# Optimization experiments

Measured on AMD Instinct MI355X. Metric: run time of the kernel, lower is better.

The kernel has to match this reference:

```python
import jax, jax.numpy as jnp
import numpy as np

DIM = 1024
HEADS = 16
DIM_HEAD = 64
INNER = HEADS * DIM_HEAD  # 1024
MLP = 4096
EPS = 1e-5


def setup_inputs() -> dict:
    key = jax.random.key(0)
    ks = jax.random.split(key, 8)
    s = lambda fan_in: 1.0 / np.sqrt(fan_in)
    return {
        "x": jax.random.normal(ks[0], (4, 2048, DIM), dtype=jnp.float32),
        "ln1_g": jnp.ones((DIM,), jnp.float32),
        "ln1_b": jnp.zeros((DIM,), jnp.float32),
        "w_qkv": jax.random.normal(ks[1], (DIM, 3 * INNER), jnp.float32) * s(DIM),
        "w_out": jax.random.normal(ks[2], (INNER, DIM), jnp.float32) * s(INNER),
        "b_out": jnp.zeros((DIM,), jnp.float32),
        "ln2_g": jnp.ones((DIM,), jnp.float32),
        "ln2_b": jnp.zeros((DIM,), jnp.float32),
        "w1": jax.random.normal(ks[3], (DIM, MLP), jnp.float32) * s(DIM),
        "b1": jnp.zeros((MLP,), jnp.float32),
        "w2": jax.random.normal(ks[4], (MLP, DIM), jnp.float32) * s(MLP),
        "b2": jnp.zeros((DIM,), jnp.float32),
    }


def _layernorm(x, g, b):
    mu = jnp.mean(x, axis=-1, keepdims=True)
    var = jnp.mean(jnp.square(x - mu), axis=-1, keepdims=True)
    return (x - mu) * jax.lax.rsqrt(var + EPS) * g + b


def _block(x, ln1_g, ln1_b, w_qkv, w_out, b_out, ln2_g, ln2_b, w1, b1, w2, b2):
    # pre-norm attention
    h = _layernorm(x, ln1_g, ln1_b)
    qkv = h @ w_qkv  # [b, n, 3*inner]
    q, k, v = jnp.split(qkv, 3, axis=-1)
    def heads(t):  # b n (h d) -> b h n d
        b, n, _ = t.shape
        return t.reshape(b, n, HEADS, DIM_HEAD).transpose(0, 2, 1, 3)
    q, k, v = heads(q), heads(k), heads(v)
    scale = DIM_HEAD ** -0.5
    dots = jnp.einsum("bhnd,bhmd->bhnm", q, k) * scale
    attn = jax.nn.softmax(dots, axis=-1)
    out = jnp.einsum("bhnm,bhmd->bhnd", attn, v)
    b, _, n, _ = out.shape
    out = out.transpose(0, 2, 1, 3).reshape(b, n, INNER)
    x = out @ w_out + b_out + x
    # pre-norm FFN
    h = _layernorm(x, ln2_g, ln2_b)
    h = jax.nn.gelu(h @ w1 + b1, approximate=False)
    return h @ w2 + b2 + x


def reference(x, ln1_g, ln1_b, w_qkv, w_out, b_out, ln2_g, ln2_b, w1, b1, w2, b2):
    return _block(x, ln1_g, ln1_b, w_qkv, w_out, b_out, ln2_g, ln2_b, w1, b1, w2, b2)
```

## Files before the change

kernel.cpp:

```cpp
#include <hip/hip_runtime.h>
#include <hip/hip_bf16.h>
#include <math.h>


typedef __bf16 bf16;
typedef __bf16 bf16x8 __attribute__((ext_vector_type(8)));
typedef __bf16 bf16x4 __attribute__((ext_vector_type(4)));
typedef float  f32x4  __attribute__((ext_vector_type(4)));
typedef unsigned int u32;

#define MFMA_16x16x32(a, b, c) __builtin_amdgcn_mfma_f32_16x16x32_bf16((a), (b), (c), 0, 0, 0)

__device__ __forceinline__ void gl_lds16(const void* g, void* l) {
    __builtin_amdgcn_global_load_lds(
        (const __attribute__((address_space(1))) u32*)g,
        (__attribute__((address_space(3))) u32*)l, 16, 0, 0);
}

__device__ __forceinline__ float fast_gelu(float x) {
    const float u = x * (0.7978845608028654f + 0.03567740814183f * x * x);
    const float e = __builtin_amdgcn_exp2f(u * 2.8853900817779268f);
    return x * e * __builtin_amdgcn_rcpf(e + 1.0f);
}

__global__ __launch_bounds__(256) void transpose_f32_bf16(
    const float* __restrict__ in, bf16* __restrict__ out, int R, int C)
{
    __shared__ float tile[32][33];
    const int cb = blockIdx.x * 32, rb = blockIdx.y * 32;
    const int c = threadIdx.x & 31, r0 = threadIdx.x >> 5;
#pragma unroll
    for (int i = 0; i < 4; ++i) {
        int r = r0 + i * 8;
        tile[r][c] = in[(size_t)(rb + r) * C + cb + c];
    }
    __syncthreads();
#pragma unroll
    for (int i = 0; i < 4; ++i) {
        int rr = r0 + i * 8;
        out[(size_t)(cb + rr) * R + rb + c] = (bf16)tile[c][rr];
    }
}

__global__ __launch_bounds__(256) void transpose_v(
    const bf16* __restrict__ qkv, bf16* __restrict__ VT)
{
    __shared__ float tile[32][33];
    const int tokb = blockIdx.x * 32;
    const int db   = blockIdx.y * 32;
    const int bh   = blockIdx.z;
    const int b = bh >> 4, h = bh & 15;
    const int c = threadIdx.x & 31, r0 = threadIdx.x >> 5;
#pragma unroll
    for (int i = 0; i < 4; ++i) {
        int r = r0 + i * 8;
        tile[r][c] = (float)qkv[(size_t)(b * 2048 + tokb + r) * 3072 + 2048 + h * 64 + db + c];
    }
    __syncthreads();
#pragma unroll
    for (int i = 0; i < 4; ++i) {
        int rr = r0 + i * 8;
        VT[((size_t)bh * 64 + db + rr) * 2048 + tokb + c] = (bf16)tile[c][rr];
    }
}

__global__ __launch_bounds__(256) void ln_kernel(
    const float* __restrict__ x, const float* __restrict__ g,
    const float* __restrict__ b, bf16* __restrict__ out)
{
    const int lane = threadIdx.x & 63;
    const int wv   = threadIdx.x >> 6;
    const size_t token = (size_t)blockIdx.x * 4 + wv;
    const float* xr = x + token * 1024;
    float4 v[4];
    float s = 0.f, ss = 0.f;
#pragma unroll
    for (int c = 0; c < 4; ++c) {
        v[c] = *(const float4*)(xr + c * 256 + lane * 4);
        s  += v[c].x + v[c].y + v[c].z + v[c].w;
        ss += v[c].x * v[c].x + v[c].y * v[c].y + v[c].z * v[c].z + v[c].w * v[c].w;
    }
#pragma unroll
    for (int off = 32; off > 0; off >>= 1) {
        s  += __shfl_xor(s, off);
        ss += __shfl_xor(ss, off);
    }
    const float mu  = s * (1.0f / 1024.0f);
    const float var = ss * (1.0f / 1024.0f) - mu * mu;
    const float rs  = rsqrtf(var + 1e-5f);
    bf16* orow = out + token * 1024;
#pragma unroll
    for (int c = 0; c < 4; ++c) {
        float4 gg = *(const float4*)(g + c * 256 + lane * 4);
        float4 bb = *(const float4*)(b + c * 256 + lane * 4);
        bf16x4 o;
        o[0] = (bf16)((v[c].x - mu) * rs * gg.x + bb.x);
        o[1] = (bf16)((v[c].y - mu) * rs * gg.y + bb.y);
        o[2] = (bf16)((v[c].z - mu) * rs * gg.z + bb.z);
        o[3] = (bf16)((v[c].w - mu) * rs * gg.w + bb.w);
        *(bf16x4*)(orow + c * 256 + lane * 4) = o;
    }
}

template <int EPI>
__global__ __launch_bounds__(256, 4) void gemm_bt(
    const bf16* __restrict__ A, const bf16* __restrict__ Bt,
    const float* __restrict__ bias, const float* __restrict__ resid,
    void* __restrict__ outp, int M, int N, int K)
{
    __shared__ __align__(16) bf16 sA[128 * 64];
    __shared__ __align__(16) bf16 sB[128 * 64];

    const int tid  = threadIdx.x;
    const int lane = tid & 63;
    const int wv   = tid >> 6;
    const int quad = lane >> 4;
    const int l16  = lane & 15;

    const int id  = blockIdx.x;
    const int xcd = id & 7, j = id >> 3;
    const int M0 = (xcd * 8 + (j & 7)) * 128;
    const int N0 = (j >> 3) * 128;

    const int wm = (wv >> 1) * 64;
    const int wn = (wv & 1) * 64;

    f32x4 acc[4][4] = {};

    const bf16* paG[4];
    const bf16* pbG[4];
#pragma unroll
    for (int c = 0; c < 4; ++c) {
        const int f = c * 256 + tid;
        const int row = f >> 3;
        const int gch = (f & 7) ^ (row & 7);
        paG[c] = A  + (size_t)(M0 + row) * K + gch * 8;
        pbG[c] = Bt + (size_t)(N0 + row) * K + gch * 8;
    }

    const int sw = l16 & 7;

    for (int k0 = 0; k0 < K; k0 += 64) {
        __syncthreads();
#pragma unroll
        for (int c = 0; c < 4; ++c) {
            const int f8 = (c * 256 + tid) * 8;
            gl_lds16(paG[c] + k0, sA + f8);
            gl_lds16(pbG[c] + k0, sB + f8);
        }
        __syncthreads();

#pragma unroll
        for (int s = 0; s < 2; ++s) {
            const int chp = (s * 4 + quad) ^ sw;
            bf16x8 af[4], bfr[4];
#pragma unroll
            for (int t = 0; t < 4; ++t)
                af[t] = *(const bf16x8*)(sA + ((wm + t * 16 + l16) << 6) + chp * 8);
#pragma unroll
            for (int t = 0; t < 4; ++t)
                bfr[t] = *(const bf16x8*)(sB + ((wn + t * 16 + l16) << 6) + chp * 8);
#pragma unroll
            for (int tm = 0; tm < 4; ++tm)
#pragma unroll
                for (int tn = 0; tn < 4; ++tn)
                    acc[tm][tn] = MFMA_16x16x32(bfr[tn], af[tm], acc[tm][tn]);
        }
    }

#pragma unroll
    for (int tm = 0; tm < 4; ++tm) {
        const int row = M0 + wm + tm * 16 + l16;
#pragma unroll
        for (int tn = 0; tn < 4; ++tn) {
            const int col = N0 + wn + tn * 16 + quad * 4;
            const size_t idx = (size_t)row * N + col;
            const f32x4 v = acc[tm][tn];
            if (EPI == 0) {
                bf16x4 o;
#pragma unroll
                for (int r = 0; r < 4; ++r) o[r] = (bf16)v[r];
                *(bf16x4*)((bf16*)outp + idx) = o;
            } else if (EPI == 1) {
                const f32x4 b4 = *(const f32x4*)(bias + col);
                const f32x4 r4 = *(const f32x4*)(resid + idx);
                *(f32x4*)((float*)outp + idx) = v + b4 + r4;
            } else {
                const f32x4 b4 = *(const f32x4*)(bias + col);
                bf16x4 o;
#pragma unroll
                for (int r = 0; r < 4; ++r) o[r] = (bf16)fast_gelu(v[r] + b4[r]);
                *(bf16x4*)((bf16*)outp + idx) = o;
            }
        }
    }
}

__global__ __launch_bounds__(256, 4) void attn_kernel(
    const bf16* __restrict__ qkv, const bf16* __restrict__ VT,
    bf16* __restrict__ attn_out)
{
    __shared__ __align__(16) bf16 sK[4096];
    __shared__ __align__(16) bf16 sV[4096];
    __shared__ __align__(16) bf16 sP[4][32][72];

    const int bh = blockIdx.y, b = bh >> 4, h = bh & 15;
    const int tid = threadIdx.x, lane = tid & 63, wv = tid >> 6;
    const int quad = lane >> 4, l16 = lane & 15;
    const size_t tok0 = (size_t)b * 2048;
    const int q0 = blockIdx.x * 128 + wv * 32;

    bf16x8 qf[2][2];
#pragma unroll
    for (int mi = 0; mi < 2; ++mi)
#pragma unroll
        for (int c = 0; c < 2; ++c) {
            bf16x8 t = *(const bf16x8*)(qkv + (tok0 + q0 + mi * 16 + l16) * 3072 + h * 64 + c * 32 + quad * 8);
#pragma unroll
            for (int j = 0; j < 8; ++j) t[j] = (bf16)((float)t[j] * 0.18033688011112042f);
            qf[mi][c] = t;
        }

    f32x4 o[2][4] = {};
    float l[2][4] = {};

    const int fA = tid, fB = tid + 256;
    const int cKA = fA >> 8, keyA = (fA >> 2) & 63, qcA = fA & 3;
    const int cKB = fB >> 8, keyB = (fB >> 2) & 63, qcB = fB & 3;
    const int dVA = fA >> 3, ccA = fA & 7;
    const int dVB = fB >> 3, ccB = fB & 7;
    const bf16* Kb = qkv + 1024 + h * 64;
    const bf16* Vb = VT + (size_t)bh * 64 * 2048;

    for (int kt = 0; kt < 32; ++kt) {
        const int kb = kt * 64;
        __syncthreads();
        gl_lds16(Kb + (tok0 + kb + keyA) * 3072 + cKA * 32 + ((qcA ^ (keyA & 3)) * 8), sK + fA * 8);
        gl_lds16(Kb + (tok0 + kb + keyB) * 3072 + cKB * 32 + ((qcB ^ (keyB & 3)) * 8), sK + fB * 8);
        gl_lds16(Vb + (size_t)dVA * 2048 + kb + ((ccA ^ (dVA & 7)) * 8), sV + fA * 8);
        gl_lds16(Vb + (size_t)dVB * 2048 + kb + ((ccB ^ (dVB & 7)) * 8), sV + fB * 8);
        __syncthreads();

        f32x4 s[2][4];
#pragma unroll
        for (int ct = 0; ct < 4; ++ct) {
            const int key = ct * 16 + l16;
            const int ch = quad ^ (l16 & 3);
            bf16x8 k0 = *(const bf16x8*)(sK + (key * 4 + ch) * 8);
            bf16x8 k1 = *(const bf16x8*)(sK + (256 + key * 4 + ch) * 8);
#pragma unroll
            for (int mi = 0; mi < 2; ++mi) {
                f32x4 z = {};
                z = MFMA_16x16x32(qf[mi][0], k0, z);
                z = MFMA_16x16x32(qf[mi][1], k1, z);
                s[mi][ct] = z;
            }
        }
#pragma unroll
        for (int mi = 0; mi < 2; ++mi)
#pragma unroll
            for (int ct = 0; ct < 4; ++ct)
#pragma unroll
                for (int r = 0; r < 4; ++r) {
                    const float p = __builtin_amdgcn_exp2f(s[mi][ct][r]);
                    l[mi][r] += p;
                    sP[wv][mi * 16 + quad * 4 + r][ct * 16 + l16] = (bf16)p;
                }
        bf16x8 vb[4][2];
#pragma unroll
        for (int dt = 0; dt < 4; ++dt) {
            const int d = dt * 16 + l16;
            vb[dt][0] = *(const bf16x8*)(sV + (d * 8 + (quad ^ (l16 & 7))) * 8);
            vb[dt][1] = *(const bf16x8*)(sV + (d * 8 + ((quad + 4) ^ (l16 & 7))) * 8);
        }
#pragma unroll
        for (int mi = 0; mi < 2; ++mi) {
            bf16x8 p0 = *(const bf16x8*)&sP[wv][mi * 16 + l16][quad * 8];
            bf16x8 p1 = *(const bf16x8*)&sP[wv][mi * 16 + l16][32 + quad * 8];
#pragma unroll
            for (int dt = 0; dt < 4; ++dt) {
                o[mi][dt] = MFMA_16x16x32(p0, vb[dt][0], o[mi][dt]);
                o[mi][dt] = MFMA_16x16x32(p1, vb[dt][1], o[mi][dt]);
            }
        }
    }

#pragma unroll
    for (int mi = 0; mi < 2; ++mi) {
        float rl[4];
#pragma unroll
        for (int r = 0; r < 4; ++r) {
            float t = l[mi][r];
            t += __shfl_xor(t, 1); t += __shfl_xor(t, 2);
            t += __shfl_xor(t, 4); t += __shfl_xor(t, 8);
            rl[r] = 1.0f / t;
        }
#pragma unroll
        for (int dt = 0; dt < 4; ++dt)
#pragma unroll
            for (int r = 0; r < 4; ++r) {
                const size_t tok = tok0 + q0 + mi * 16 + quad * 4 + r;
                attn_out[tok * 1024 + h * 64 + dt * 16 + l16] = (bf16)(o[mi][dt][r] * rl[r]);
            }
    }
}

extern "C" void kernel_launch(void* const* d_in, const int* in_sizes, int n_in,
                              void* d_out, int out_size, void* d_ws, size_t ws_size,
                              hipStream_t stream)
{
    const float* x     = (const float*)d_in[0];
    const float* ln1_g = (const float*)d_in[1];
    const float* ln1_b = (const float*)d_in[2];
    const float* w_qkv = (const float*)d_in[3];
    const float* w_out = (const float*)d_in[4];
    const float* b_out = (const float*)d_in[5];
    const float* ln2_g = (const float*)d_in[6];
    const float* ln2_b = (const float*)d_in[7];
    const float* w1    = (const float*)d_in[8];
    const float* b1    = (const float*)d_in[9];
    const float* w2    = (const float*)d_in[10];
    const float* b2    = (const float*)d_in[11];
    float* out = (float*)d_out;

    char* ws = (char*)d_ws;
    bf16*  h      = (bf16*)(ws);
    bf16*  big    = (bf16*)(ws + 16777216);
    bf16*  attn_o = (bf16*)(ws + 83886080);
    float* x_mid  = (float*)(ws + 100663296);
    bf16*  VT     = (bf16*)(ws + 100663296);
    bf16*  wT_qkv = (bf16*)(ws + 134217728);
    bf16*  wT_out = (bf16*)(ws + 140509184);
    bf16*  wT_1   = (bf16*)(ws + 142606336);
    bf16*  wT_2   = (bf16*)(ws + 150994944);

    transpose_f32_bf16<<<dim3(3072/32, 1024/32), 256, 0, stream>>>(w_qkv, wT_qkv, 1024, 3072);
    transpose_f32_bf16<<<dim3(1024/32, 1024/32), 256, 0, stream>>>(w_out, wT_out, 1024, 1024);
    transpose_f32_bf16<<<dim3(4096/32, 1024/32), 256, 0, stream>>>(w1,    wT_1,   1024, 4096);
    transpose_f32_bf16<<<dim3(1024/32, 4096/32), 256, 0, stream>>>(w2,    wT_2,   4096, 1024);

    ln_kernel<<<2048, 256, 0, stream>>>(x, ln1_g, ln1_b, h);

    gemm_bt<0><<<64 * 24, 256, 0, stream>>>(h, wT_qkv, nullptr, nullptr, big, 8192, 3072, 1024);

    transpose_v<<<dim3(64, 2, 64), 256, 0, stream>>>(big, VT);

    attn_kernel<<<dim3(16, 64), 256, 0, stream>>>(big, VT, attn_o);

    gemm_bt<1><<<64 * 8, 256, 0, stream>>>(attn_o, wT_out, b_out, x, x_mid, 8192, 1024, 1024);

    ln_kernel<<<2048, 256, 0, stream>>>(x_mid, ln2_g, ln2_b, h);

    gemm_bt<2><<<64 * 32, 256, 0, stream>>>(h, wT_1, b1, nullptr, big, 8192, 4096, 1024);

    gemm_bt<1><<<64 * 8, 256, 0, stream>>>(big, wT_2, b2, x_mid, out, 8192, 1024, 4096);
}
```

Before: 489.4 us.

## Keep attention probabilities in registers via transposed QK^T and permlane swaps

The QK^T MFMA now runs with K as the A operand, so each lane holds scores for one query across keys. The exponentiated probabilities are packed to bf16 and rearranged with v_permlane32/16_swap into the A-operand layout for the PV MFMA. This removes the shared-memory staging buffer for P and its write/read round trip. It also adds s_setprio around the MFMA sections, and changes the row-sum reduction to a single per-lane sum broadcast with shuffles, at the cost of more register pressure and reliance on gfx950-specific permlane instructions.

```diff
diff --git a/kernel.cpp b/kernel.cpp
--- a/kernel.cpp
+++ b/kernel.cpp
@@ -6,15 +6,25 @@
 typedef __bf16 bf16;
 typedef __bf16 bf16x8 __attribute__((ext_vector_type(8)));
 typedef __bf16 bf16x4 __attribute__((ext_vector_type(4)));
+typedef __bf16 bf16x2 __attribute__((ext_vector_type(2)));
 typedef float  f32x4  __attribute__((ext_vector_type(4)));
 typedef unsigned int u32;
+typedef u32 u32x4 __attribute__((ext_vector_type(4)));
 
 #define MFMA_16x16x32(a, b, c) __builtin_amdgcn_mfma_f32_16x16x32_bf16((a), (b), (c), 0, 0, 0)
+
+#define SWAP32(x, y) asm("v_permlane32_swap_b32 %0, %1" : "+v"(x), "+v"(y))
+#define SWAP16(x, y) asm("v_permlane16_swap_b32 %0, %1" : "+v"(x), "+v"(y))
 
 __device__ __forceinline__ void gl_lds16(const void* g, void* l) {
     __builtin_amdgcn_global_load_lds(
         (const __attribute__((address_space(1))) u32*)g,
         (__attribute__((address_space(3))) u32*)l, 16, 0, 0);
+}
+
+__device__ __forceinline__ u32 pack_bf16x2(float a, float b) {
+    bf16x2 t; t[0] = (bf16)a; t[1] = (bf16)b;
+    return __builtin_bit_cast(u32, t);
 }
 
 __device__ __forceinline__ float fast_gelu(float x) {
@@ -202,7 +212,6 @@
 {
     __shared__ __align__(16) bf16 sK[4096];
     __shared__ __align__(16) bf16 sV[4096];
-    __shared__ __align__(16) bf16 sP[4][32][72];
 
     const int bh = blockIdx.y, b = bh >> 4, h = bh & 15;
     const int tid = threadIdx.x, lane = tid & 63, wv = tid >> 6;
@@ -222,7 +231,7 @@
         }
 
     f32x4 o[2][4] = {};
-    float l[2][4] = {};
+    float lsum[2] = {0.f, 0.f};
 
     const int fA = tid, fB = tid + 256;
     const int cKA = fA >> 8, keyA = (fA >> 2) & 63, qcA = fA & 3;
@@ -241,7 +250,8 @@
         gl_lds16(Vb + (size_t)dVB * 2048 + kb + ((ccB ^ (dVB & 7)) * 8), sV + fB * 8);
         __syncthreads();
 
-        f32x4 s[2][4];
+        u32 w[2][4][2];
+        __builtin_amdgcn_s_setprio(1);
 #pragma unroll
         for (int ct = 0; ct < 4; ++ct) {
             const int key = ct * 16 + l16;
@@ -251,50 +261,61 @@
 #pragma unroll
             for (int mi = 0; mi < 2; ++mi) {
                 f32x4 z = {};
-                z = MFMA_16x16x32(qf[mi][0], k0, z);
-                z = MFMA_16x16x32(qf[mi][1], k1, z);
-                s[mi][ct] = z;
-            }
-        }
-#pragma unroll
-        for (int mi = 0; mi < 2; ++mi)
-#pragma unroll
-            for (int ct = 0; ct < 4; ++ct)
-#pragma unroll
-                for (int r = 0; r < 4; ++r) {
-                    const float p = __builtin_amdgcn_exp2f(s[mi][ct][r]);
-                    l[mi][r] += p;
-                    sP[wv][mi * 16 + quad * 4 + r][ct * 16 + l16] = (bf16)p;
-                }
-        bf16x8 vb[4][2];
+                z = MFMA_16x16x32(k0, qf[mi][0], z);
+                z = MFMA_16x16x32(k1, qf[mi][1], z);
+                float p0 = __builtin_amdgcn_exp2f(z[0]);
+                float p1 = __builtin_amdgcn_exp2f(z[1]);
+                float p2 = __builtin_amdgcn_exp2f(z[2]);
+                float p3 = __builtin_amdgcn_exp2f(z[3]);
+                lsum[mi] += (p0 + p1) + (p2 + p3);
+                w[mi][ct][0] = pack_bf16x2(p0, p1);
+                w[mi][ct][1] = pack_bf16x2(p2, p3);
+            }
+        }
+        __builtin_amdgcn_s_setprio(0);
+
+        bf16x8 pa[2][2];
+#pragma unroll
+        for (int mi = 0; mi < 2; ++mi) {
+            u32 pw0[4], pw1[4];
+#pragma unroll
+            for (int c2 = 0; c2 < 2; ++c2) {
+                u32 x = w[mi][0][c2], y = w[mi][1][c2];
+                SWAP32(x, y); SWAP16(x, y);
+                pw0[c2] = x; pw0[2 + c2] = y;
+                u32 x2 = w[mi][2][c2], y2 = w[mi][3][c2];
+                SWAP32(x2, y2); SWAP16(x2, y2);
+                pw1[c2] = x2; pw1[2 + c2] = y2;
+            }
+            u32x4 t0 = {pw0[0], pw0[1], pw0[2], pw0[3]};
+            u32x4 t1 = {pw1[0], pw1[1], pw1[2], pw1[3]};
+            pa[mi][0] = __builtin_bit_cast(bf16x8, t0);
+            pa[mi][1] = __builtin_bit_cast(bf16x8, t1);
+        }
+
+        __builtin_amdgcn_s_setprio(1);
 #pragma unroll
         for (int dt = 0; dt < 4; ++dt) {
             const int d = dt * 16 + l16;
-            vb[dt][0] = *(const bf16x8*)(sV + (d * 8 + (quad ^ (l16 & 7))) * 8);
-            vb[dt][1] = *(const bf16x8*)(sV + (d * 8 + ((quad + 4) ^ (l16 & 7))) * 8);
-        }
-#pragma unroll
-        for (int mi = 0; mi < 2; ++mi) {
-            bf16x8 p0 = *(const bf16x8*)&sP[wv][mi * 16 + l16][quad * 8];
-            bf16x8 p1 = *(const bf16x8*)&sP[wv][mi * 16 + l16][32 + quad * 8];
-#pragma unroll
-            for (int dt = 0; dt < 4; ++dt) {
-                o[mi][dt] = MFMA_16x16x32(p0, vb[dt][0], o[mi][dt]);
-                o[mi][dt] = MFMA_16x16x32(p1, vb[dt][1], o[mi][dt]);
-            }
-        }
+            bf16x8 v0 = *(const bf16x8*)(sV + (d * 8 + (quad ^ (l16 & 7))) * 8);
+            bf16x8 v1 = *(const bf16x8*)(sV + (d * 8 + ((quad + 4) ^ (l16 & 7))) * 8);
+#pragma unroll
+            for (int mi = 0; mi < 2; ++mi) {
+                o[mi][dt] = MFMA_16x16x32(pa[mi][0], v0, o[mi][dt]);
+                o[mi][dt] = MFMA_16x16x32(pa[mi][1], v1, o[mi][dt]);
+            }
+        }
+        __builtin_amdgcn_s_setprio(0);
     }
 
 #pragma unroll
     for (int mi = 0; mi < 2; ++mi) {
+        float t = lsum[mi];
+        t += __shfl_xor(t, 16);
+        t += __shfl_xor(t, 32);
         float rl[4];
 #pragma unroll
-        for (int r = 0; r < 4; ++r) {
-            float t = l[mi][r];
-            t += __shfl_xor(t, 1); t += __shfl_xor(t, 2);
-            t += __shfl_xor(t, 4); t += __shfl_xor(t, 8);
-            rl[r] = 1.0f / t;
-        }
+        for (int r = 0; r < 4; ++r) rl[r] = 1.0f / __shfl(t, quad * 4 + r);
 #pragma unroll
         for (int dt = 0; dt < 4; ++dt)
 #pragma unroll
```

Result: no change. 492.7 us (+0.7%).
